# Performance work log

Measured on AMD Instinct MI355X. Metric: run time of the kernel, lower is better.

## Reference

```python
import jax, jax.numpy as jnp
import numpy as np
import math

TANH_CLIP = 10.0
MAX_TIME = 1440.0


def setup_inputs() -> dict:
    key = jax.random.key(0)
    ks = jax.random.split(key, 16)
    B, N, D, S = 1024, 512, 128, 3
    sc = 1.0 / math.sqrt(D)
    inp = {
        'node_emb': jax.random.normal(ks[0], (B, N, D), jnp.float32),
        'W_last': jax.random.normal(ks[1], (D, D), jnp.float32) * sc,
        'W_first': jax.random.normal(ks[2], (D, D), jnp.float32) * sc,
        'W_graph': jax.random.normal(ks[3], (D, D), jnp.float32) * sc,
        'W_visited': jax.random.normal(ks[4], (D, D), jnp.float32) * sc,
        'W_key': jax.random.normal(ks[5], (D, D), jnp.float32) * sc,
        'W_state': jax.random.normal(ks[6], (S, D), jnp.float32) * sc,
        'b_state': jnp.zeros((D,), jnp.float32),
        'current_time': jax.random.uniform(ks[7], (B, 1), jnp.float32) * MAX_TIME,
        'used_capacity': jax.random.uniform(ks[8], (B, 1), jnp.float32),
        'vehicle_capacity': jnp.ones((B, 1), jnp.float32),
        'travel_time_matrix': jax.random.uniform(ks[9], (N, N), jnp.float32) * MAX_TIME,
        'current_node': jax.random.randint(ks[10], (B, 1), 0, N, jnp.int32),
        'previous_action': jax.random.randint(ks[11], (B, 1), 0, N, jnp.int32),
        'first_node': jax.random.randint(ks[12], (B,), 0, N, jnp.int32),
        'visited': jax.random.randint(ks[13], (B, N), 0, 2, jnp.int32).astype(bool),
        'action_mask': jax.random.randint(ks[14], (B, N), 0, 2, jnp.int32).astype(bool),
        'i': jax.random.randint(ks[15], (B, 1), 0, 2 * N, jnp.int32),
        'h3_indices': jax.random.randint(jax.random.fold_in(key, 99), (B, N), 0, N, jnp.int32),
    }
    return inp


def reference(node_emb, W_last, W_first, W_graph, W_visited, W_key, W_state, b_state,
              current_time, used_capacity, vehicle_capacity, travel_time_matrix,
              current_node, previous_action, first_node, visited, action_mask, i, h3_indices):
    B, N, D = node_emb.shape
    barange = jnp.arange(B)

    # precompute (cache)
    K = jnp.einsum('bnd,de->bne', node_emb, W_key)          # [B,N,D]
    graph_emb = node_emb.mean(axis=1)                        # [B,D]

    # first-node bookkeeping
    cur = current_node[:, 0]
    prev = previous_action[:, 0]
    left_depot = (prev == 0) & (cur != 0)
    fn = jnp.where(left_depot, cur, first_node)
    fn = jnp.where(cur == 0, jnp.zeros_like(fn), fn)

    # context gathers
    h_current = node_emb[barange, cur]                       # [B,D]
    h_first = node_emb[barange, fn]                          # [B,D]
    vf = visited.astype(node_emb.dtype)                      # [B,N]
    vcount = jnp.clip(vf.sum(axis=-1, keepdims=True), 1.0)
    h_visited = jnp.einsum('bn,bnd->bd', vf, node_emb) / vcount

    # scalar state features
    remaining_cap = (vehicle_capacity - used_capacity)[:, 0]
    ct = current_time[:, 0] / MAX_TIME
    step_feat = i[:, 0].astype(node_emb.dtype) / (N * 2)
    state_feats = jnp.stack([remaining_cap, ct, step_feat], axis=-1)  # [B,3]

    q = (h_current @ W_last + h_first @ W_first + graph_emb @ W_graph
         + h_visited @ W_visited + state_feats @ W_state + b_state)   # [B,D]

    score = jnp.einsum('bd,bnd->bn', q, K) / math.sqrt(D)   # [B,N]

    # travel-time bias (shared 2D matrix)
    cur_h3 = h3_indices[barange, cur]                        # [B]
    row = travel_time_matrix[cur_h3]                         # [B,N]
    travel = jnp.take_along_axis(row, h3_indices, axis=1)    # [B,N]
    score = score - travel / MAX_TIME / math.sqrt(2.0)

    score = TANH_CLIP * jnp.tanh(score / TANH_CLIP)
    score = jnp.where(action_mask, score, -1e8)
    return jax.nn.log_softmax(score, axis=-1)
```

## Files before the change

kernel.cpp:

```cpp
#include <hip/hip_runtime.h>
#include <math.h>

#define NB 1024
#define NN 512
#define ND 128
#define NT 512

typedef float f4 __attribute__((ext_vector_type(4)));

__device__ __forceinline__ f4 ldnt(const float* p) {
    return __builtin_nontemporal_load(reinterpret_cast<const f4*>(p));
}

#define QSC   15.875f
#define DQSC  (8.0f / 127.0f)

__global__ __launch_bounds__(NT, 4) void darp_fused(
    const float* __restrict__ node_emb,
    const float* __restrict__ W_last,
    const float* __restrict__ W_first,
    const float* __restrict__ W_graph,
    const float* __restrict__ W_visited,
    const float* __restrict__ W_key,
    const float* __restrict__ W_state,
    const float* __restrict__ b_state,
    const float* __restrict__ current_time,
    const float* __restrict__ used_capacity,
    const float* __restrict__ vehicle_capacity,
    const float* __restrict__ ttm,
    const int* __restrict__ current_node,
    const int* __restrict__ previous_action,
    const int* __restrict__ first_node,
    const int* __restrict__ visited,
    const int* __restrict__ action_mask,
    const int* __restrict__ step_i,
    const int* __restrict__ h3_indices,
    float* __restrict__ out)
{
    const int b    = blockIdx.x;
    const int t    = threadIdx.x;
    const int wave = t >> 6;
    const int lane = t & 63;
    const int l5   = t & 31;
    const int strm = t >> 5;

    __shared__ char  smem_u[8192] __attribute__((aligned(16)));
    __shared__ unsigned long long smask[8];
    __shared__ float smean[ND];
    __shared__ float svis[ND];
    __shared__ float shcur[ND];
    __shared__ float shfirst[ND];
    __shared__ float qs[ND];
    __shared__ float qp[ND] __attribute__((aligned(16)));
    __shared__ float sred[16];
    __shared__ float s_scal[4];
    __shared__ float s_qsum;
    __shared__ unsigned int tile[NN * 32];

    float4 (*sgh)[32] = reinterpret_cast<float4(*)[32]>(smem_u);
    float4 (*svh)[32] = reinterpret_cast<float4(*)[32]>(smem_u + 4096);
    float*  scratch   = reinterpret_cast<float*>(smem_u);

    const float* nbp = node_emb + (size_t)b * NN * ND;

    int cur  = current_node[b];
    int prev = previous_action[b];
    int fn   = first_node[b];
    if (prev == 0 && cur != 0) fn = cur;
    if (cur == 0) fn = 0;

    float4 hc4, hf4;
    if (t < 32)       hc4 = *reinterpret_cast<const float4*>(nbp + (size_t)cur * ND + t * 4);
    else if (t < 64)  hf4 = *reinterpret_cast<const float4*>(nbp + (size_t)fn  * ND + (t - 32) * 4);

    {
        const int f = (visited[(size_t)b * NN + t] != 0);
        unsigned long long m = __ballot(f);
        if (lane == 0) smask[wave] = m;
        float vc = f ? 1.0f : 0.0f;
#pragma unroll
        for (int off = 32; off >= 1; off >>= 1) vc += __shfl_xor(vc, off);
        if (lane == 0) sred[wave] = vc;
    }
    __syncthreads();

    {
        const int r0 = strm * 32;
        const float* p = nbp + (size_t)r0 * ND + l5 * 4;
        const unsigned int mybits =
            (unsigned int)(smask[strm >> 1] >> ((strm & 1) * 32));
        unsigned int* tw = tile + r0 * 32;

        float4 g = make_float4(0.f, 0.f, 0.f, 0.f);
        float4 v = make_float4(0.f, 0.f, 0.f, 0.f);

        f4 xa[8], xb[8];
#pragma unroll
        for (int u = 0; u < 8; ++u) xa[u] = ldnt(p + (size_t)u * ND);
#pragma unroll
        for (int u = 0; u < 8; ++u) xb[u] = ldnt(p + (size_t)(8 + u) * ND);

#define PROC8(BUF, BASE)                                                       \
        {                                                                      \
            _Pragma("unroll")                                                  \
            for (int u = 0; u < 8; ++u) {                                      \
                const f4 X = BUF[u];                                           \
                const int k = (BASE) + u;                                      \
                const float vf = ((mybits >> k) & 1u) ? 1.0f : 0.0f;           \
                g.x += X.x; g.y += X.y; g.z += X.z; g.w += X.w;                \
                v.x = fmaf(vf, X.x, v.x); v.y = fmaf(vf, X.y, v.y);            \
                v.z = fmaf(vf, X.z, v.z); v.w = fmaf(vf, X.w, v.w);            \
                const float c0 = fmaf(X.x, QSC, 128.5f);                       \
                const float c1 = fmaf(X.y, QSC, 128.5f);                       \
                const float c2 = fmaf(X.z, QSC, 128.5f);                       \
                const float c3 = fmaf(X.w, QSC, 128.5f);                       \
                unsigned int w = __builtin_amdgcn_cvt_pk_u8_f32(c0, 0, 0u);    \
                w = __builtin_amdgcn_cvt_pk_u8_f32(c1, 1, w);                  \
                w = __builtin_amdgcn_cvt_pk_u8_f32(c2, 2, w);                  \
                w = __builtin_amdgcn_cvt_pk_u8_f32(c3, 3, w);                  \
                tw[k * 32 + (l5 ^ k)] = w;                                     \
            }                                                                  \
        }

        PROC8(xa, 0)
#pragma unroll
        for (int u = 0; u < 8; ++u) xa[u] = ldnt(p + (size_t)(16 + u) * ND);
        PROC8(xb, 8)
#pragma unroll
        for (int u = 0; u < 8; ++u) xb[u] = ldnt(p + (size_t)(24 + u) * ND);
        PROC8(xa, 16)
        PROC8(xb, 24)
#undef PROC8

        g.x += __shfl_xor(g.x, 32); g.y += __shfl_xor(g.y, 32);
        g.z += __shfl_xor(g.z, 32); g.w += __shfl_xor(g.w, 32);
        v.x += __shfl_xor(v.x, 32); v.y += __shfl_xor(v.y, 32);
        v.z += __shfl_xor(v.z, 32); v.w += __shfl_xor(v.w, 32);
        if (lane < 32) { sgh[wave][l5] = g; svh[wave][l5] = v; }
    }
    __syncthreads();

    if (t < 32)       *reinterpret_cast<float4*>(&shcur[t * 4]) = hc4;
    else if (t < 64)  *reinterpret_cast<float4*>(&shfirst[(t - 32) * 4]) = hf4;

    if (t >= 64 && t < 96) {
        const int c = t - 64;
        float4 G = sgh[0][c], V = svh[0][c];
#pragma unroll
        for (int j = 1; j < 8; ++j) {
            float4 a = sgh[j][c], d = svh[j][c];
            G.x += a.x; G.y += a.y; G.z += a.z; G.w += a.w;
            V.x += d.x; V.y += d.y; V.z += d.z; V.w += d.w;
        }
        const float invN = 1.0f / (float)NN;
        smean[c * 4 + 0] = G.x * invN; smean[c * 4 + 1] = G.y * invN;
        smean[c * 4 + 2] = G.z * invN; smean[c * 4 + 3] = G.w * invN;
        svis[c * 4 + 0] = V.x; svis[c * 4 + 1] = V.y;
        svis[c * 4 + 2] = V.z; svis[c * 4 + 3] = V.w;
    }
    if (t == 128) {
        float c = sred[0] + sred[1] + sred[2] + sred[3]
                + sred[4] + sred[5] + sred[6] + sred[7];
        s_scal[0] = 1.0f / fmaxf(c, 1.0f);
        s_scal[1] = vehicle_capacity[b] - used_capacity[b];
        s_scal[2] = current_time[b] * (1.0f / 1440.0f);
        s_scal[3] = (float)step_i[b] * (1.0f / (2.0f * (float)NN));
    }
    __syncthreads();

    {
        const int e  = t & 127;
        const int g2 = t >> 7;
        const int d0 = g2 * 32;
        float a0 = 0.f, a1 = 0.f, a2 = 0.f, a3 = 0.f;
#pragma unroll 8
        for (int dd = 0; dd < 32; ++dd) {
            int d = d0 + dd;
            a0 = fmaf(shcur[d],   W_last[d * ND + e],    a0);
            a1 = fmaf(shfirst[d], W_first[d * ND + e],   a1);
            a2 = fmaf(smean[d],   W_graph[d * ND + e],   a2);
            a3 = fmaf(svis[d],    W_visited[d * ND + e], a3);
        }
        float pacc = a0 + a1 + a2 + s_scal[0] * a3;
        if (g2 == 0) {
            pacc += b_state[e]
                  + s_scal[1] * W_state[e]
                  + s_scal[2] * W_state[ND + e]
                  + s_scal[3] * W_state[2 * ND + e];
        }
        scratch[g2 * 128 + e] = pacc;
    }
    __syncthreads();

    if (t < ND) qs[t] = scratch[t] + scratch[128 + t]
                      + scratch[256 + t] + scratch[384 + t];
    __syncthreads();

    {
        float4 qv = *reinterpret_cast<const float4*>(&qs[l5 * 4]);
#pragma unroll
        for (int it = 0; it < 8; ++it) {
            int d = it * 16 + strm;
            float4 wk = *reinterpret_cast<const float4*>(W_key + (size_t)d * ND + l5 * 4);
            float s = wk.x * qv.x + wk.y * qv.y + wk.z * qv.z + wk.w * qv.w;
            s += __shfl_xor(s, 16); s += __shfl_xor(s, 8);
            s += __shfl_xor(s, 4);  s += __shfl_xor(s, 2); s += __shfl_xor(s, 1);
            if (l5 == 0) qp[d] = s * (0.08838834764831845f * DQSC);
        }
    }
    __syncthreads();

    if (t < 64) {
        float s = qp[t] + qp[t + 64];
#pragma unroll
        for (int off = 32; off >= 1; off >>= 1) s += __shfl_xor(s, off);
        if (t == 0) s_qsum = s;
    }
    __syncthreads();

    {
        const unsigned int* tr = tile + t * 32;
        const int sw = t & 31;
        float s1 = 0.f;
#pragma unroll 8
        for (int c = 0; c < 32; ++c) {
            const unsigned int w = tr[c ^ sw];
            const float4 q4 = *reinterpret_cast<const float4*>(&qp[c * 4]);
            const float f0 = (float)(w & 0xffu);
            const float f1 = (float)((w >> 8) & 0xffu);
            const float f2 = (float)((w >> 16) & 0xffu);
            const float f3 = (float)(w >> 24);
            s1 = fmaf(f0, q4.x, s1); s1 = fmaf(f1, q4.y, s1);
            s1 = fmaf(f2, q4.z, s1); s1 = fmaf(f3, q4.w, s1);
        }
        s1 -= 128.0f * s_qsum;

        const int    cur_h3 = h3_indices[(size_t)b * NN + cur];
        const float* trow   = ttm + (size_t)cur_h3 * NN;
        const float  tscale = 1.0f / (1440.0f * 1.4142135623730951f);

        int h1 = h3_indices[(size_t)b * NN + t];
        s1 -= trow[h1] * tscale;
        s1 = 10.0f * tanhf(s1 * 0.1f);
        if (!action_mask[(size_t)b * NN + t]) s1 = -1e8f;

        float m = s1;
#pragma unroll
        for (int off = 32; off >= 1; off >>= 1) m = fmaxf(m, __shfl_xor(m, off));
        if (lane == 0) sred[wave] = m;
        __syncthreads();
        float bm = fmaxf(fmaxf(fmaxf(sred[0], sred[1]), fmaxf(sred[2], sred[3])),
                         fmaxf(fmaxf(sred[4], sred[5]), fmaxf(sred[6], sred[7])));

        float es = expf(s1 - bm);
#pragma unroll
        for (int off = 32; off >= 1; off >>= 1) es += __shfl_xor(es, off);
        if (lane == 0) sred[8 + wave] = es;
        __syncthreads();
        float lse = bm + logf(sred[8]  + sred[9]  + sred[10] + sred[11]
                            + sred[12] + sred[13] + sred[14] + sred[15]);

        out[(size_t)b * NN + t] = s1 - lse;
    }
}

extern "C" void kernel_launch(void* const* d_in, const int* in_sizes, int n_in,
                              void* d_out, int out_size, void* d_ws, size_t ws_size,
                              hipStream_t stream) {
    (void)in_sizes; (void)n_in; (void)d_ws; (void)ws_size; (void)out_size;
    darp_fused<<<dim3(NB), dim3(NT), 0, stream>>>(
        (const float*)d_in[0],
        (const float*)d_in[1],
        (const float*)d_in[2],
        (const float*)d_in[3],
        (const float*)d_in[4],
        (const float*)d_in[5],
        (const float*)d_in[6],
        (const float*)d_in[7],
        (const float*)d_in[8],
        (const float*)d_in[9],
        (const float*)d_in[10],
        (const float*)d_in[11],
        (const int*)d_in[12],
        (const int*)d_in[13],
        (const int*)d_in[14],
        (const int*)d_in[15],
        (const int*)d_in[16],
        (const int*)d_in[17],
        (const int*)d_in[18],
        (float*)d_out);
}
```

Before: 86.06 us.

## Split column-sum reduction into separate pre-kernel and drop nontemporal loads

Moves the graph-mean and visited-weighted sum over node_emb into a separate, highly parallel kernel (8 chunks per batch) that writes partials to workspace, and the main kernel reads them instead of computing them inline. Nontemporal loads are replaced with normal loads, presumably so the second pass over node_emb can hit in the L2/last-level cache. The cost is reading node_emb twice (256MB each) plus an extra launch, in exchange for a shorter critical path in the score kernel.

```diff
diff --git a/kernel.cpp b/kernel.cpp
--- a/kernel.cpp
+++ b/kernel.cpp
@@ -1,21 +1,79 @@
 #include <hip/hip_runtime.h>
 #include <math.h>
 
-#define NB 1024
 #define NN 512
 #define ND 128
-#define NT 512
 
 typedef float f4 __attribute__((ext_vector_type(4)));
-
-__device__ __forceinline__ f4 ldnt(const float* p) {
-    return __builtin_nontemporal_load(reinterpret_cast<const f4*>(p));
-}
 
 #define QSC   15.875f
 #define DQSC  (8.0f / 127.0f)
-
-__global__ __launch_bounds__(NT, 4) void darp_fused(
+#define TSCALE (1.0f / (1440.0f * 1.4142135623730951f))
+#define WSP_STRIDE 272
+
+__global__ __launch_bounds__(256, 6) void k1_colsum(
+    const float* __restrict__ node_emb,
+    const int*   __restrict__ visited,
+    float*       __restrict__ wsp)
+{
+    const int bid = blockIdx.x;
+    const int b   = bid >> 3;
+    const int ch  = bid & 7;
+    const int t   = threadIdx.x;
+    const int l5  = t & 31;
+    const int grp = t >> 5;
+
+    __shared__ float  svisf[64];
+    __shared__ float4 sg[8][32];
+    __shared__ float4 sv[8][32];
+    __shared__ float  scnt;
+
+    const int rbase = ch * 64;
+    if (t < 64) svisf[t] = visited[(size_t)b * NN + rbase + t] ? 1.f : 0.f;
+    __syncthreads();
+
+    const float* p = node_emb + (size_t)b * NN * ND + (size_t)rbase * ND + t * 4;
+    f4 x[8];
+#pragma unroll
+    for (int u = 0; u < 8; ++u)
+        x[u] = *reinterpret_cast<const f4*>(p + (size_t)u * 1024);
+
+    float4 g = make_float4(0.f, 0.f, 0.f, 0.f);
+    float4 v = make_float4(0.f, 0.f, 0.f, 0.f);
+#pragma unroll
+    for (int u = 0; u < 8; ++u) {
+        const float vf = svisf[u * 8 + grp];
+        g.x += x[u].x; g.y += x[u].y; g.z += x[u].z; g.w += x[u].w;
+        v.x = fmaf(vf, x[u].x, v.x); v.y = fmaf(vf, x[u].y, v.y);
+        v.z = fmaf(vf, x[u].z, v.z); v.w = fmaf(vf, x[u].w, v.w);
+    }
+    sg[grp][l5] = g;
+    sv[grp][l5] = v;
+
+    if (t < 64) {
+        float vc = svisf[t];
+#pragma unroll
+        for (int off = 32; off >= 1; off >>= 1) vc += __shfl_xor(vc, off);
+        if (t == 0) scnt = vc;
+    }
+    __syncthreads();
+
+    if (t < 32) {
+        float4 G = sg[0][t], V = sv[0][t];
+#pragma unroll
+        for (int j = 1; j < 8; ++j) {
+            float4 a = sg[j][t], d = sv[j][t];
+            G.x += a.x; G.y += a.y; G.z += a.z; G.w += a.w;
+            V.x += d.x; V.y += d.y; V.z += d.z; V.w += d.w;
+        }
+        float* o = wsp + (size_t)bid * WSP_STRIDE;
+        *reinterpret_cast<float4*>(o + t * 4)       = G;
+        *reinterpret_cast<float4*>(o + 128 + t * 4) = V;
+        if (t == 0) o[256] = scnt;
+    }
+}
+
+__global__ __launch_bounds__(512, 4) void k2_score(
     const float* __restrict__ node_emb,
     const float* __restrict__ W_last,
     const float* __restrict__ W_first,
@@ -31,10 +89,10 @@
     const int* __restrict__ current_node,
     const int* __restrict__ previous_action,
     const int* __restrict__ first_node,
-    const int* __restrict__ visited,
     const int* __restrict__ action_mask,
     const int* __restrict__ step_i,
     const int* __restrict__ h3_indices,
+    const float* __restrict__ wsp,
     float* __restrict__ out)
 {
     const int b    = blockIdx.x;
@@ -44,22 +102,17 @@
     const int l5   = t & 31;
     const int strm = t >> 5;
 
-    __shared__ char  smem_u[8192] __attribute__((aligned(16)));
-    __shared__ unsigned long long smask[8];
     __shared__ float smean[ND];
     __shared__ float svis[ND];
     __shared__ float shcur[ND];
     __shared__ float shfirst[ND];
     __shared__ float qs[ND];
     __shared__ float qp[ND] __attribute__((aligned(16)));
+    __shared__ float scratch[512];
     __shared__ float sred[16];
     __shared__ float s_scal[4];
     __shared__ float s_qsum;
     __shared__ unsigned int tile[NN * 32];
-
-    float4 (*sgh)[32] = reinterpret_cast<float4(*)[32]>(smem_u);
-    float4 (*svh)[32] = reinterpret_cast<float4(*)[32]>(smem_u + 4096);
-    float*  scratch   = reinterpret_cast<float*>(smem_u);
 
     const float* nbp = node_emb + (size_t)b * NN * ND;
 
@@ -69,36 +122,38 @@
     if (prev == 0 && cur != 0) fn = cur;
     if (cur == 0) fn = 0;
 
+    float pg[8], pv[8];
+    if (t < 128) {
+#pragma unroll
+        for (int k = 0; k < 8; ++k) {
+            const float* o = wsp + (size_t)(b * 8 + k) * WSP_STRIDE;
+            pg[k] = o[t];
+            pv[k] = o[128 + t];
+        }
+    }
     float4 hc4, hf4;
-    if (t < 32)       hc4 = *reinterpret_cast<const float4*>(nbp + (size_t)cur * ND + t * 4);
-    else if (t < 64)  hf4 = *reinterpret_cast<const float4*>(nbp + (size_t)fn  * ND + (t - 32) * 4);
-
-    {
-        const int f = (visited[(size_t)b * NN + t] != 0);
-        unsigned long long m = __ballot(f);
-        if (lane == 0) smask[wave] = m;
-        float vc = f ? 1.0f : 0.0f;
-#pragma unroll
-        for (int off = 32; off >= 1; off >>= 1) vc += __shfl_xor(vc, off);
-        if (lane == 0) sred[wave] = vc;
-    }
-    __syncthreads();
+    if (t >= 128 && t < 160)
+        hc4 = *reinterpret_cast<const float4*>(nbp + (size_t)cur * ND + (t - 128) * 4);
+    else if (t >= 160 && t < 192)
+        hf4 = *reinterpret_cast<const float4*>(nbp + (size_t)fn * ND + (t - 160) * 4);
+    float cnt = 0.f, r_cap = 0.f, r_ctm = 0.f, r_sf = 0.f;
+    if (t == 192) {
+#pragma unroll
+        for (int k = 0; k < 8; ++k) cnt += wsp[(size_t)(b * 8 + k) * WSP_STRIDE + 256];
+        r_cap = vehicle_capacity[b] - used_capacity[b];
+        r_ctm = current_time[b] * (1.0f / 1440.0f);
+        r_sf  = (float)step_i[b] * (1.0f / (2.0f * (float)NN));
+    }
 
     {
         const int r0 = strm * 32;
         const float* p = nbp + (size_t)r0 * ND + l5 * 4;
-        const unsigned int mybits =
-            (unsigned int)(smask[strm >> 1] >> ((strm & 1) * 32));
-        unsigned int* tw = tile + r0 * 32;
-
-        float4 g = make_float4(0.f, 0.f, 0.f, 0.f);
-        float4 v = make_float4(0.f, 0.f, 0.f, 0.f);
 
         f4 xa[8], xb[8];
 #pragma unroll
-        for (int u = 0; u < 8; ++u) xa[u] = ldnt(p + (size_t)u * ND);
-#pragma unroll
-        for (int u = 0; u < 8; ++u) xb[u] = ldnt(p + (size_t)(8 + u) * ND);
+        for (int u = 0; u < 8; ++u) xa[u] = *reinterpret_cast<const f4*>(p + (size_t)u * ND);
+#pragma unroll
+        for (int u = 0; u < 8; ++u) xb[u] = *reinterpret_cast<const f4*>(p + (size_t)(8 + u) * ND);
 
 #define PROC8(BUF, BASE)                                                       \
         {                                                                      \
@@ -106,10 +161,6 @@
             for (int u = 0; u < 8; ++u) {                                      \
                 const f4 X = BUF[u];                                           \
                 const int k = (BASE) + u;                                      \
-                const float vf = ((mybits >> k) & 1u) ? 1.0f : 0.0f;           \
-                g.x += X.x; g.y += X.y; g.z += X.z; g.w += X.w;                \
-                v.x = fmaf(vf, X.x, v.x); v.y = fmaf(vf, X.y, v.y);            \
-                v.z = fmaf(vf, X.z, v.z); v.w = fmaf(vf, X.w, v.w);            \
                 const float c0 = fmaf(X.x, QSC, 128.5f);                       \
                 const float c1 = fmaf(X.y, QSC, 128.5f);                       \
                 const float c2 = fmaf(X.z, QSC, 128.5f);                       \
@@ -118,53 +169,36 @@
                 w = __builtin_amdgcn_cvt_pk_u8_f32(c1, 1, w);                  \
                 w = __builtin_amdgcn_cvt_pk_u8_f32(c2, 2, w);                  \
                 w = __builtin_amdgcn_cvt_pk_u8_f32(c3, 3, w);                  \
-                tw[k * 32 + (l5 ^ k)] = w;                                     \
+                tile[(r0 + k) * 32 + (l5 ^ (k & 31))] = w;                     \
             }                                                                  \
         }
 
         PROC8(xa, 0)
 #pragma unroll
-        for (int u = 0; u < 8; ++u) xa[u] = ldnt(p + (size_t)(16 + u) * ND);
+        for (int u = 0; u < 8; ++u) xa[u] = *reinterpret_cast<const f4*>(p + (size_t)(16 + u) * ND);
         PROC8(xb, 8)
 #pragma unroll
-        for (int u = 0; u < 8; ++u) xb[u] = ldnt(p + (size_t)(24 + u) * ND);
+        for (int u = 0; u < 8; ++u) xb[u] = *reinterpret_cast<const f4*>(p + (size_t)(24 + u) * ND);
         PROC8(xa, 16)
         PROC8(xb, 24)
 #undef PROC8
-
-        g.x += __shfl_xor(g.x, 32); g.y += __shfl_xor(g.y, 32);
-        g.z += __shfl_xor(g.z, 32); g.w += __shfl_xor(g.w, 32);
-        v.x += __shfl_xor(v.x, 32); v.y += __shfl_xor(v.y, 32);
-        v.z += __shfl_xor(v.z, 32); v.w += __shfl_xor(v.w, 32);
-        if (lane < 32) { sgh[wave][l5] = g; svh[wave][l5] = v; }
-    }
-    __syncthreads();
-
-    if (t < 32)       *reinterpret_cast<float4*>(&shcur[t * 4]) = hc4;
-    else if (t < 64)  *reinterpret_cast<float4*>(&shfirst[(t - 32) * 4]) = hf4;
-
-    if (t >= 64 && t < 96) {
-        const int c = t - 64;
-        float4 G = sgh[0][c], V = svh[0][c];
-#pragma unroll
-        for (int j = 1; j < 8; ++j) {
-            float4 a = sgh[j][c], d = svh[j][c];
-            G.x += a.x; G.y += a.y; G.z += a.z; G.w += a.w;
-            V.x += d.x; V.y += d.y; V.z += d.z; V.w += d.w;
-        }
-        const float invN = 1.0f / (float)NN;
-        smean[c * 4 + 0] = G.x * invN; smean[c * 4 + 1] = G.y * invN;
-        smean[c * 4 + 2] = G.z * invN; smean[c * 4 + 3] = G.w * invN;
-        svis[c * 4 + 0] = V.x; svis[c * 4 + 1] = V.y;
-        svis[c * 4 + 2] = V.z; svis[c * 4 + 3] = V.w;
-    }
-    if (t == 128) {
-        float c = sred[0] + sred[1] + sred[2] + sred[3]
-                + sred[4] + sred[5] + sred[6] + sred[7];
-        s_scal[0] = 1.0f / fmaxf(c, 1.0f);
-        s_scal[1] = vehicle_capacity[b] - used_capacity[b];
-        s_scal[2] = current_time[b] * (1.0f / 1440.0f);
-        s_scal[3] = (float)step_i[b] * (1.0f / (2.0f * (float)NN));
+    }
+    __syncthreads();
+
+    if (t < 128) {
+        float G = pg[0] + pg[1] + pg[2] + pg[3] + pg[4] + pg[5] + pg[6] + pg[7];
+        float V = pv[0] + pv[1] + pv[2] + pv[3] + pv[4] + pv[5] + pv[6] + pv[7];
+        smean[t] = G * (1.0f / (float)NN);
+        svis[t]  = V;
+    } else if (t < 160) {
+        *reinterpret_cast<float4*>(&shcur[(t - 128) * 4]) = hc4;
+    } else if (t < 192) {
+        *reinterpret_cast<float4*>(&shfirst[(t - 160) * 4]) = hf4;
+    } else if (t == 192) {
+        s_scal[0] = 1.0f / fmaxf(cnt, 1.0f);
+        s_scal[1] = r_cap;
+        s_scal[2] = r_ctm;
+        s_scal[3] = r_sf;
     }
     __syncthreads();
 
@@ -226,21 +260,17 @@
         for (int c = 0; c < 32; ++c) {
             const unsigned int w = tr[c ^ sw];
             const float4 q4 = *reinterpret_cast<const float4*>(&qp[c * 4]);
-            const float f0 = (float)(w & 0xffu);
-            const float f1 = (float)((w >> 8) & 0xffu);
-            const float f2 = (float)((w >> 16) & 0xffu);
-            const float f3 = (float)(w >> 24);
-            s1 = fmaf(f0, q4.x, s1); s1 = fmaf(f1, q4.y, s1);
-            s1 = fmaf(f2, q4.z, s1); s1 = fmaf(f3, q4.w, s1);
+            s1 = fmaf((float)(w & 0xffu),         q4.x, s1);
+            s1 = fmaf((float)((w >> 8) & 0xffu),  q4.y, s1);
+            s1 = fmaf((float)((w >> 16) & 0xffu), q4.z, s1);
+            s1 = fmaf((float)(w >> 24),           q4.w, s1);
         }
         s1 -= 128.0f * s_qsum;
 
         const int    cur_h3 = h3_indices[(size_t)b * NN + cur];
         const float* trow   = ttm + (size_t)cur_h3 * NN;
-        const float  tscale = 1.0f / (1440.0f * 1.4142135623730951f);
-
-        int h1 = h3_indices[(size_t)b * NN + t];
-        s1 -= trow[h1] * tscale;
+        const int h1 = h3_indices[(size_t)b * NN + t];
+        s1 -= trow[h1] * TSCALE;
         s1 = 10.0f * tanhf(s1 * 0.1f);
         if (!action_mask[(size_t)b * NN + t]) s1 = -1e8f;
 
@@ -267,9 +297,15 @@
 extern "C" void kernel_launch(void* const* d_in, const int* in_sizes, int n_in,
                               void* d_out, int out_size, void* d_ws, size_t ws_size,
                               hipStream_t stream) {
-    (void)in_sizes; (void)n_in; (void)d_ws; (void)ws_size; (void)out_size;
-    darp_fused<<<dim3(NB), dim3(NT), 0, stream>>>(
-        (const float*)d_in[0],
+    (void)in_sizes; (void)n_in; (void)ws_size; (void)out_size;
+    const float* node_emb   = (const float*)d_in[0];
+    const int*   visited    = (const int*)d_in[15];
+    float*       wsp        = (float*)d_ws;
+
+    k1_colsum<<<dim3(1024 * 8), dim3(256), 0, stream>>>(node_emb, visited, wsp);
+
+    k2_score<<<dim3(1024), dim3(512), 0, stream>>>(
+        node_emb,
         (const float*)d_in[1],
         (const float*)d_in[2],
         (const float*)d_in[3],
@@ -284,9 +320,9 @@
         (const int*)d_in[12],
         (const int*)d_in[13],
         (const int*)d_in[14],
-        (const int*)d_in[15],
         (const int*)d_in[16],
         (const int*)d_in[17],
         (const int*)d_in[18],
+        wsp,
         (float*)d_out);
 }
```

Measured after the change: 137.6 us. 1.6x slower.
